# Kernel optimization log

Hardware: AMD Instinct MI355X
Metric: run time of the kernel (lower is better)

## Reference

```python
import jax, jax.numpy as jnp
import numpy as np

B, S, E, H = 4, 2048, 768, 12
D = E // H  # 64


def setup_inputs() -> dict:
    key = jax.random.key(0)
    ks = jax.random.split(key, 9)
    scale = 0.02
    return {
        "hidden_states": jax.random.normal(ks[0], (B, S, E), dtype=jnp.float32),
        "attention_mask": jax.random.normal(ks[1], (B, 1, 1, S), dtype=jnp.float32),
        "domain_attn_mask": jax.random.normal(ks[2], (B, 1, S, S), dtype=jnp.float32),
        "Wq": jax.random.normal(ks[3], (E, E), dtype=jnp.float32) * scale,
        "bq": jax.random.normal(ks[4], (E,), dtype=jnp.float32) * scale,
        "Wk": jax.random.normal(ks[5], (E, E), dtype=jnp.float32) * scale,
        "bk": jax.random.normal(ks[6], (E,), dtype=jnp.float32) * scale,
        "Wv": jax.random.normal(ks[7], (E, E), dtype=jnp.float32) * scale,
        "bv": jax.random.normal(ks[8], (E,), dtype=jnp.float32) * scale,
    }


def _split_heads(x):
    # [B,S,E] -> [B,H,S,D]
    b, s, _ = x.shape
    return x.reshape(b, s, H, D).transpose(0, 2, 1, 3)


def reference(hidden_states, attention_mask, domain_attn_mask, Wq, bq, Wk, bk, Wv, bv):
    # nn.Linear applies x @ W.T + b
    q = _split_heads(hidden_states @ Wq.T + bq)  # [B,H,S,D]
    k = _split_heads(hidden_states @ Wk.T + bk)
    v = _split_heads(hidden_states @ Wv.T + bv)

    inv_sqrt_d = 1.0 / (D ** 0.5)
    scores = jnp.einsum('bhqd,bhkd->bhqk', q, k) * inv_sqrt_d  # [B,H,S,S]
    scores = scores + attention_mask + domain_attn_mask  # two additive masks
    probs = jax.nn.softmax(scores, axis=-1)  # dropout prob = 0.0 (eval)
    ctx = jnp.einsum('bhqk,bhkd->bhqd', probs, v)  # [B,H,S,D]
    ctx = ctx.transpose(0, 2, 1, 3).reshape(hidden_states.shape[0], hidden_states.shape[1], E)
    return ctx
```

## Files before the change

### kernel.cpp

```cpp
#include <hip/hip_runtime.h>


typedef __bf16 bf16x8 __attribute__((ext_vector_type(8)));
typedef float f32x4 __attribute__((ext_vector_type(4)));
typedef unsigned short u16x8 __attribute__((ext_vector_type(8)));

#define MFMA16(a, b, c) __builtin_amdgcn_mfma_f32_16x16x32_bf16((a), (b), (c), 0, 0, 0)

__device__ __forceinline__ unsigned short f32_to_bf16(float f) {
    unsigned int u = __builtin_bit_cast(unsigned int, f);
    u += 0x7FFFu + ((u >> 16) & 1u);
    return (unsigned short)(u >> 16);
}

__device__ __forceinline__ void gload_lds16(const void* g, void* l) {
    __builtin_amdgcn_global_load_lds(
        (const __attribute__((address_space(1))) void*)g,
        (__attribute__((address_space(3))) void*)l, 16, 0, 0);
}

__global__ __launch_bounds__(256) void cvt_f32_bf16(const float* __restrict__ src,
                                                    unsigned short* __restrict__ dst, int n4) {
    int i = blockIdx.x * 256 + threadIdx.x;
    if (i < n4) {
        const float4 v = reinterpret_cast<const float4*>(src)[i];
        ushort4 o;
        o.x = f32_to_bf16(v.x);
        o.y = f32_to_bf16(v.y);
        o.z = f32_to_bf16(v.z);
        o.w = f32_to_bf16(v.w);
        reinterpret_cast<ushort4*>(dst)[i] = o;
    }
}

__global__ __launch_bounds__(256) void cvt_weights(const float* __restrict__ Wq,
                                                   const float* __restrict__ Wk,
                                                   const float* __restrict__ Wv,
                                                   unsigned short* __restrict__ Wb) {
    int i = blockIdx.x * 256 + threadIdx.x;
    const float* src;
    int local = i;
    if (i < 147456) {
        src = Wq;
    } else if (i < 294912) {
        src = Wk; local = i - 147456;
    } else {
        src = Wv; local = i - 294912;
    }
    const float4 v = reinterpret_cast<const float4*>(src)[local];
    ushort4 o;
    o.x = f32_to_bf16(v.x);
    o.y = f32_to_bf16(v.y);
    o.z = f32_to_bf16(v.z);
    o.w = f32_to_bf16(v.w);
    reinterpret_cast<ushort4*>(Wb)[i] = o;
}

__global__ __launch_bounds__(256) void qkv_gemm(const unsigned short* __restrict__ Xb,
                                                const unsigned short* __restrict__ Wb,
                                                const float* __restrict__ bq,
                                                const float* __restrict__ bk,
                                                const float* __restrict__ bv,
                                                unsigned short* __restrict__ Qb,
                                                unsigned short* __restrict__ Kb,
                                                unsigned short* __restrict__ Vb) {
    const int K = 768;
    __shared__ __align__(16) unsigned short Abuf[128 * 32];
    __shared__ __align__(16) unsigned short Bbuf[128 * 32];

    const int lane = threadIdx.x & 63;
    const int w    = threadIdx.x >> 6;
    const int col  = lane & 15;
    const int g    = lane >> 4;
    const int m0 = blockIdx.y * 128;
    const int n0 = blockIdx.x * 128;
    const int wm = w >> 1, wn = w & 1;

    const int srow = w * 16 + (lane >> 2);
    const int scol = (lane & 3) * 8;
    const unsigned short* gA0 = Xb + (size_t)(m0 + srow) * K + scol;
    const unsigned short* gA1 = gA0 + (size_t)64 * K;
    const unsigned short* gB0 = Wb + (size_t)(n0 + srow) * K + scol;
    const unsigned short* gB1 = gB0 + (size_t)64 * K;
    char* lA0 = (char*)Abuf + w * 1024;
    char* lA1 = (char*)Abuf + 4096 + w * 1024;
    char* lB0 = (char*)Bbuf + w * 1024;
    char* lB1 = (char*)Bbuf + 4096 + w * 1024;

    f32x4 acc[4][4] = {};
    for (int k0 = 0; k0 < K; k0 += 32) {
        __syncthreads();
        gload_lds16(gA0 + k0, lA0);
        gload_lds16(gA1 + k0, lA1);
        gload_lds16(gB0 + k0, lB0);
        gload_lds16(gB1 + k0, lB1);
        __syncthreads();
        bf16x8 a[4], bfr[4];
#pragma unroll
        for (int t = 0; t < 4; ++t) {
            a[t]   = *reinterpret_cast<const bf16x8*>(Abuf + (wm * 64 + t * 16 + col) * 32 + 8 * g);
            bfr[t] = *reinterpret_cast<const bf16x8*>(Bbuf + (wn * 64 + t * 16 + col) * 32 + 8 * g);
        }
#pragma unroll
        for (int mi = 0; mi < 4; ++mi)
#pragma unroll
            for (int ni = 0; ni < 4; ++ni)
                acc[mi][ni] = MFMA16(a[mi], bfr[ni], acc[mi][ni]);
    }

    const int which = n0 / 768;
    const float* bias = (which == 0) ? bq : (which == 1) ? bk : bv;
    const float scale = (which == 0) ? 0.125f : 1.0f;
    unsigned short* dst = (which == 0) ? Qb : (which == 1) ? Kb : Vb;

#pragma unroll
    for (int ni = 0; ni < 4; ++ni) {
        const int n = n0 + wn * 64 + ni * 16 + col;
        const int e = n - which * 768;
        const int h = e >> 6;
        const int d = e & 63;
        const float bb = bias[e];
#pragma unroll
        for (int mi = 0; mi < 4; ++mi)
#pragma unroll
            for (int i = 0; i < 4; ++i) {
                const int m   = m0 + wm * 64 + mi * 16 + 4 * g + i;
                const int bh  = (m >> 11) * 12 + h;
                const int srw = m & 2047;
                const float v = (acc[mi][ni][i] + bb) * scale;
                dst[((size_t)bh * 2048 + srw) * 64 + d] = f32_to_bf16(v);
            }
    }
}

__global__ __launch_bounds__(256) void transpose_v(const unsigned short* __restrict__ Vb,
                                                   unsigned short* __restrict__ Vt) {
    __shared__ unsigned short T[64][72];
    const int bh = blockIdx.y;
    const int s0 = blockIdx.x * 64;
    const int t  = threadIdx.x;
    const int r  = t >> 2;
    const int c0 = (t & 3) * 16;

    const unsigned short* src = Vb + ((size_t)bh * 2048 + s0 + r) * 64 + c0;
    u16x8 a = *reinterpret_cast<const u16x8*>(src);
    u16x8 b = *reinterpret_cast<const u16x8*>(src + 8);
#pragma unroll
    for (int j = 0; j < 8; ++j) {
        T[c0 + j][r]     = a[j];
        T[c0 + 8 + j][r] = b[j];
    }
    __syncthreads();
    unsigned short* dstp = Vt + ((size_t)bh * 64 + r) * 2048 + s0 + c0;
    *reinterpret_cast<u16x8*>(dstp)     = *reinterpret_cast<const u16x8*>(&T[r][c0]);
    *reinterpret_cast<u16x8*>(dstp + 8) = *reinterpret_cast<const u16x8*>(&T[r][c0 + 8]);
}

__global__ __launch_bounds__(256, 3) void attn_kernel(const unsigned short* __restrict__ Qb,
                                                      const unsigned short* __restrict__ Kb,
                                                      const unsigned short* __restrict__ Vt,
                                                      const float* __restrict__ amask,
                                                      const float* __restrict__ dmask,
                                                      float* __restrict__ out) {
    const int S = 2048, H = 12;
    const int lane = threadIdx.x & 63;
    const int w    = threadIdx.x >> 6;
    const int col  = lane & 15;
    const int g    = lane >> 4;

    const int phys    = blockIdx.x;
    const int logical = (phys & 7) * 96 + (phys >> 3);
    const int bh = logical >> 4;
    const int qt = logical & 15;
    const int b  = bh / H;
    const int h  = bh % H;
    const int q0 = qt * 128 + w * 32;

    __shared__ __align__(16) unsigned short Kl[2][4096];
    __shared__ __align__(16) unsigned short Vl[2][4096];
    __shared__ __align__(16) unsigned short Pl[4][32][72];

    bf16x8 qf[2][2];
#pragma unroll
    for (int qg = 0; qg < 2; ++qg)
#pragma unroll
        for (int kst = 0; kst < 2; ++kst)
            qf[qg][kst] = *reinterpret_cast<const bf16x8*>(
                Qb + ((size_t)bh * S + q0 + qg * 16 + col) * 64 + kst * 32 + 8 * g);

    f32x4 octx[2][4] = {};
    float m_run[2] = {-1e30f, -1e30f}, l_run[2] = {0.0f, 0.0f};

    const float* dmr0 = dmask + (size_t)b * S * S + (size_t)(q0 + col) * S;
    const float* dmr1 = dmr0 + (size_t)16 * S;
    const float* amr  = amask + (size_t)b * S;

#define STAGE(buf, KV)                                                              \
    {                                                                               \
        _Pragma("unroll")                                                           \
        for (int c = 0; c < 2; ++c) {                                               \
            const int base = w * 2048 + c * 1024;                      \
            const int o    = base + (lane << 4);                                    \
            const int row  = o >> 7;                                                \
            const int slot = (o >> 4) & 7;                                          \
            const int chunk = slot ^ (row & 7);                                     \
            gload_lds16((const char*)(Kb + ((size_t)bh * S + (KV) + row) * 64) + chunk * 16, \
                        (char*)&Kl[buf][0] + base);                                 \
            gload_lds16((const char*)(Vt + ((size_t)bh * 64 + row) * S + (KV)) + chunk * 16, \
                        (char*)&Vl[buf][0] + base);                                 \
        }                                                                           \
    }

    STAGE(0, 0)
    __syncthreads();

    int cur = 0;
    for (int t = 0; t < 32; ++t) {
        const int kv = t * 64;
        if (t + 1 < 32) STAGE(cur ^ 1, kv + 64)

        f32x4 dm[2][4], am4[4];
#pragma unroll
        for (int s = 0; s < 4; ++s) {
            dm[0][s] = *reinterpret_cast<const f32x4*>(dmr0 + kv + s * 16 + 4 * g);
            dm[1][s] = *reinterpret_cast<const f32x4*>(dmr1 + kv + s * 16 + 4 * g);
            am4[s]   = *reinterpret_cast<const f32x4*>(amr  + kv + s * 16 + 4 * g);
        }

        f32x4 sc[2][4] = {};
#pragma unroll
        for (int s = 0; s < 4; ++s) {
            const int row = s * 16 + col;
#pragma unroll
            for (int kst = 0; kst < 2; ++kst) {
                bf16x8 kf = *reinterpret_cast<const bf16x8*>(
                    (const char*)&Kl[cur][0] + row * 128 + (((g + 4 * kst) ^ (col & 7)) << 4));
                sc[0][s] = MFMA16(kf, qf[0][kst], sc[0][s]);
                sc[1][s] = MFMA16(kf, qf[1][kst], sc[1][s]);
            }
        }

#pragma unroll
        for (int qg = 0; qg < 2; ++qg) {
#pragma unroll
            for (int s = 0; s < 4; ++s) sc[qg][s] += dm[qg][s] + am4[s];
            float tm = sc[qg][0][0];
#pragma unroll
            for (int s = 0; s < 4; ++s)
#pragma unroll
                for (int i = 0; i < 4; ++i) tm = fmaxf(tm, sc[qg][s][i]);
            tm = fmaxf(tm, __shfl_xor(tm, 16));
            tm = fmaxf(tm, __shfl_xor(tm, 32));
            const bool grow = tm > m_run[qg];
            const float mn = fmaxf(m_run[qg], tm);
            float rs = 0.0f;
#pragma unroll
            for (int s = 0; s < 4; ++s)
#pragma unroll
                for (int i = 0; i < 4; ++i) {
                    const float p = __expf(sc[qg][s][i] - mn);
                    sc[qg][s][i] = p;
                    rs += p;
                }
            rs += __shfl_xor(rs, 16);
            rs += __shfl_xor(rs, 32);
            if (__any(grow)) {
                const float sf = __expf(m_run[qg] - mn);
                l_run[qg] = l_run[qg] * sf + rs;
                m_run[qg] = mn;
#pragma unroll
                for (int ds_ = 0; ds_ < 4; ++ds_) octx[qg][ds_] *= sf;
            } else {
                l_run[qg] += rs;
            }
#pragma unroll
            for (int s = 0; s < 4; ++s) {
                ushort4 u;
                u.x = f32_to_bf16(sc[qg][s][0]);
                u.y = f32_to_bf16(sc[qg][s][1]);
                u.z = f32_to_bf16(sc[qg][s][2]);
                u.w = f32_to_bf16(sc[qg][s][3]);
                *reinterpret_cast<ushort4*>(&Pl[w][qg * 16 + col][s * 16 + 4 * g]) = u;
            }
        }

        bf16x8 pb[2][2];
#pragma unroll
        for (int qg = 0; qg < 2; ++qg)
#pragma unroll
            for (int kst = 0; kst < 2; ++kst)
                pb[qg][kst] = *reinterpret_cast<const bf16x8*>(
                    &Pl[w][qg * 16 + col][kst * 32 + 8 * g]);
#pragma unroll
        for (int ds_ = 0; ds_ < 4; ++ds_) {
            const int row = ds_ * 16 + col;
#pragma unroll
            for (int kst = 0; kst < 2; ++kst) {
                bf16x8 vf = *reinterpret_cast<const bf16x8*>(
                    (const char*)&Vl[cur][0] + row * 128 + (((g + 4 * kst) ^ (col & 7)) << 4));
                octx[0][ds_] = MFMA16(vf, pb[0][kst], octx[0][ds_]);
                octx[1][ds_] = MFMA16(vf, pb[1][kst], octx[1][ds_]);
            }
        }

        __syncthreads();
        cur ^= 1;
    }

#pragma unroll
    for (int qg = 0; qg < 2; ++qg) {
        const float inv = 1.0f / l_run[qg];
        const size_t ob = ((size_t)b * S + q0 + qg * 16 + col) * 768 + h * 64;
#pragma unroll
        for (int ds_ = 0; ds_ < 4; ++ds_) {
            f32x4 o = octx[qg][ds_] * inv;
            *reinterpret_cast<f32x4*>(out + ob + ds_ * 16 + 4 * g) = o;
        }
    }
#undef STAGE
}

extern "C" void kernel_launch(void* const* d_in, const int* in_sizes, int n_in,
                              void* d_out, int out_size, void* d_ws, size_t ws_size,
                              hipStream_t stream) {
    const float* hidden = (const float*)d_in[0];
    const float* amask  = (const float*)d_in[1];
    const float* dmask  = (const float*)d_in[2];
    const float* Wq     = (const float*)d_in[3];
    const float* bq     = (const float*)d_in[4];
    const float* Wk     = (const float*)d_in[5];
    const float* bk     = (const float*)d_in[6];
    const float* Wv     = (const float*)d_in[7];
    const float* bv     = (const float*)d_in[8];
    float* out = (float*)d_out;

    unsigned short* Xb = (unsigned short*)d_ws;
    unsigned short* Wb = Xb + 6291456;
    unsigned short* Qb = Wb + 1769472;
    unsigned short* Kb = Qb + 6291456;
    unsigned short* Vb = Kb + 6291456;
    unsigned short* Vt = Xb;

    cvt_f32_bf16<<<6144, 256, 0, stream>>>(hidden, Xb, 1572864);
    cvt_weights<<<1728, 256, 0, stream>>>(Wq, Wk, Wv, Wb);
    qkv_gemm<<<dim3(18, 64), 256, 0, stream>>>(Xb, Wb, bq, bk, bv, Qb, Kb, Vb);
    transpose_v<<<dim3(32, 48), 256, 0, stream>>>(Vb, Vt);
    attn_kernel<<<768, 256, 0, stream>>>(Qb, Kb, Vt, amask, dmask, out);
}
```

Before: 318.1 us.

## Rework attention to 8 waves per block with exp2 softmax and deeper GEMM K tile

The attention kernel now runs 8 waves of 16 query rows each instead of 4 waves of 32, which lowers registers per wave and raises occupancy. Softmax uses a raw v_exp_f32 in base 2: log2(e) is folded into the Q scale and the mask add. MFMA sections are wrapped in s_setprio. The QKV GEMM moves to a 64-wide K tile with XOR-swizzled LDS to halve barriers and reduce bank conflicts. Each wave now reuses every loaded K/V fragment for half as many MFMAs, so LDS read traffic per MFMA rises.

Result: slower. 362.6 us (+14.0%).

```diff
diff --git a/kernel.cpp b/kernel.cpp
--- a/kernel.cpp
+++ b/kernel.cpp
@@ -2,10 +2,17 @@
 
 
 typedef __bf16 bf16x8 __attribute__((ext_vector_type(8)));
+typedef __bf16 bf16x4 __attribute__((ext_vector_type(4)));
 typedef float f32x4 __attribute__((ext_vector_type(4)));
 typedef unsigned short u16x8 __attribute__((ext_vector_type(8)));
 
 #define MFMA16(a, b, c) __builtin_amdgcn_mfma_f32_16x16x32_bf16((a), (b), (c), 0, 0, 0)
+
+__device__ __forceinline__ float exp2_fast(float x) {
+    float r;
+    asm("v_exp_f32 %0, %1" : "=v"(r) : "v"(x));
+    return r;
+}
 
 __device__ __forceinline__ unsigned short f32_to_bf16(float f) {
     unsigned int u = __builtin_bit_cast(unsigned int, f);
@@ -65,8 +72,8 @@
                                                 unsigned short* __restrict__ Kb,
                                                 unsigned short* __restrict__ Vb) {
     const int K = 768;
-    __shared__ __align__(16) unsigned short Abuf[128 * 32];
-    __shared__ __align__(16) unsigned short Bbuf[128 * 32];
+    __shared__ __align__(16) unsigned short Abuf[128 * 64];
+    __shared__ __align__(16) unsigned short Bbuf[128 * 64];
 
     const int lane = threadIdx.x & 63;
     const int w    = threadIdx.x >> 6;
@@ -76,41 +83,43 @@
     const int n0 = blockIdx.x * 128;
     const int wm = w >> 1, wn = w & 1;
 
-    const int srow = w * 16 + (lane >> 2);
-    const int scol = (lane & 3) * 8;
-    const unsigned short* gA0 = Xb + (size_t)(m0 + srow) * K + scol;
-    const unsigned short* gA1 = gA0 + (size_t)64 * K;
-    const unsigned short* gB0 = Wb + (size_t)(n0 + srow) * K + scol;
-    const unsigned short* gB1 = gB0 + (size_t)64 * K;
-    char* lA0 = (char*)Abuf + w * 1024;
-    char* lA1 = (char*)Abuf + 4096 + w * 1024;
-    char* lB0 = (char*)Bbuf + w * 1024;
-    char* lB1 = (char*)Bbuf + 4096 + w * 1024;
+    const int lrow   = lane >> 3;
+    const int lchunk = (lane & 7) ^ (lrow & 7);
+    const unsigned short* gA = Xb + (size_t)(m0 + w * 32 + lrow) * K + lchunk * 8;
+    const unsigned short* gB = Wb + (size_t)(n0 + w * 32 + lrow) * K + lchunk * 8;
 
     f32x4 acc[4][4] = {};
-    for (int k0 = 0; k0 < K; k0 += 32) {
+    for (int k0 = 0; k0 < K; k0 += 64) {
         __syncthreads();
-        gload_lds16(gA0 + k0, lA0);
-        gload_lds16(gA1 + k0, lA1);
-        gload_lds16(gB0 + k0, lB0);
-        gload_lds16(gB1 + k0, lB1);
+#pragma unroll
+        for (int c = 0; c < 4; ++c) {
+            gload_lds16(gA + (size_t)(c * 8) * K + k0, (char*)Abuf + w * 4096 + c * 1024);
+            gload_lds16(gB + (size_t)(c * 8) * K + k0, (char*)Bbuf + w * 4096 + c * 1024);
+        }
         __syncthreads();
-        bf16x8 a[4], bfr[4];
-#pragma unroll
-        for (int t = 0; t < 4; ++t) {
-            a[t]   = *reinterpret_cast<const bf16x8*>(Abuf + (wm * 64 + t * 16 + col) * 32 + 8 * g);
-            bfr[t] = *reinterpret_cast<const bf16x8*>(Bbuf + (wn * 64 + t * 16 + col) * 32 + 8 * g);
-        }
-#pragma unroll
-        for (int mi = 0; mi < 4; ++mi)
-#pragma unroll
-            for (int ni = 0; ni < 4; ++ni)
-                acc[mi][ni] = MFMA16(a[mi], bfr[ni], acc[mi][ni]);
+#pragma unroll
+        for (int kst = 0; kst < 2; ++kst) {
+            bf16x8 a[4], bfr[4];
+#pragma unroll
+            for (int t = 0; t < 4; ++t) {
+                const int ra = wm * 64 + t * 16 + col;
+                const int rb = wn * 64 + t * 16 + col;
+                a[t]   = *reinterpret_cast<const bf16x8*>(
+                    (const char*)Abuf + ra * 128 + (((g + 4 * kst) ^ (ra & 7)) << 4));
+                bfr[t] = *reinterpret_cast<const bf16x8*>(
+                    (const char*)Bbuf + rb * 128 + (((g + 4 * kst) ^ (rb & 7)) << 4));
+            }
+#pragma unroll
+            for (int mi = 0; mi < 4; ++mi)
+#pragma unroll
+                for (int ni = 0; ni < 4; ++ni)
+                    acc[mi][ni] = MFMA16(a[mi], bfr[ni], acc[mi][ni]);
+        }
     }
 
     const int which = n0 / 768;
     const float* bias = (which == 0) ? bq : (which == 1) ? bk : bv;
-    const float scale = (which == 0) ? 0.125f : 1.0f;
+    const float scale = (which == 0) ? 0.18033688011112042f : 1.0f;
     unsigned short* dst = (which == 0) ? Qb : (which == 1) ? Kb : Vb;
 
 #pragma unroll
@@ -156,13 +165,14 @@
     *reinterpret_cast<u16x8*>(dstp + 8) = *reinterpret_cast<const u16x8*>(&T[r][c0 + 8]);
 }
 
-__global__ __launch_bounds__(256, 3) void attn_kernel(const unsigned short* __restrict__ Qb,
+__global__ __launch_bounds__(512, 6) void attn_kernel(const unsigned short* __restrict__ Qb,
                                                       const unsigned short* __restrict__ Kb,
                                                       const unsigned short* __restrict__ Vt,
                                                       const float* __restrict__ amask,
                                                       const float* __restrict__ dmask,
                                                       float* __restrict__ out) {
     const int S = 2048, H = 12;
+    const float L2E = 1.4426950408889634f;
     const int lane = threadIdx.x & 63;
     const int w    = threadIdx.x >> 6;
     const int col  = lane & 15;
@@ -174,41 +184,36 @@
     const int qt = logical & 15;
     const int b  = bh / H;
     const int h  = bh % H;
-    const int q0 = qt * 128 + w * 32;
+    const int q0 = qt * 128 + w * 16;
+    const int q  = q0 + col;
 
     __shared__ __align__(16) unsigned short Kl[2][4096];
     __shared__ __align__(16) unsigned short Vl[2][4096];
-    __shared__ __align__(16) unsigned short Pl[4][32][72];
-
-    bf16x8 qf[2][2];
-#pragma unroll
-    for (int qg = 0; qg < 2; ++qg)
-#pragma unroll
-        for (int kst = 0; kst < 2; ++kst)
-            qf[qg][kst] = *reinterpret_cast<const bf16x8*>(
-                Qb + ((size_t)bh * S + q0 + qg * 16 + col) * 64 + kst * 32 + 8 * g);
-
-    f32x4 octx[2][4] = {};
-    float m_run[2] = {-1e30f, -1e30f}, l_run[2] = {0.0f, 0.0f};
-
-    const float* dmr0 = dmask + (size_t)b * S * S + (size_t)(q0 + col) * S;
-    const float* dmr1 = dmr0 + (size_t)16 * S;
-    const float* amr  = amask + (size_t)b * S;
-
+    __shared__ __align__(16) unsigned short Pl[8][16][72];
+
+    bf16x8 qf[2];
+#pragma unroll
+    for (int kst = 0; kst < 2; ++kst)
+        qf[kst] = *reinterpret_cast<const bf16x8*>(
+            Qb + ((size_t)bh * S + q) * 64 + kst * 32 + 8 * g);
+
+    f32x4 octx[4] = {};
+    float m_run = -1e30f, l_run = 0.0f;
+
+    const float* dmr = dmask + (size_t)b * S * S + (size_t)q * S;
+    const float* amr = amask + (size_t)b * S;
+
+    const int lrow   = lane >> 3;
+    const int lchunk = (lane & 7) ^ (lrow & 7);
 #define STAGE(buf, KV)                                                              \
     {                                                                               \
-        _Pragma("unroll")                                                           \
-        for (int c = 0; c < 2; ++c) {                                               \
-            const int base = w * 2048 + c * 1024;                      \
-            const int o    = base + (lane << 4);                                    \
-            const int row  = o >> 7;                                                \
-            const int slot = (o >> 4) & 7;                                          \
-            const int chunk = slot ^ (row & 7);                                     \
-            gload_lds16((const char*)(Kb + ((size_t)bh * S + (KV) + row) * 64) + chunk * 16, \
-                        (char*)&Kl[buf][0] + base);                                 \
-            gload_lds16((const char*)(Vt + ((size_t)bh * 64 + row) * S + (KV)) + chunk * 16, \
-                        (char*)&Vl[buf][0] + base);                                 \
-        }                                                                           \
+        const int base = w * 1024;                                                  \
+        gload_lds16((const char*)(Kb + ((size_t)bh * S + (KV) + w * 8 + lrow) * 64) \
+                        + lchunk * 16,                                              \
+                    (char*)&Kl[buf][0] + base);                                     \
+        gload_lds16((const char*)(Vt + ((size_t)bh * 64 + w * 8 + lrow) * S + (KV)) \
+                        + lchunk * 16,                                              \
+                    (char*)&Vl[buf][0] + base);                                     \
     }
 
     STAGE(0, 0)
@@ -219,15 +224,13 @@
         const int kv = t * 64;
         if (t + 1 < 32) STAGE(cur ^ 1, kv + 64)
 
-        f32x4 dm[2][4], am4[4];
-#pragma unroll
-        for (int s = 0; s < 4; ++s) {
-            dm[0][s] = *reinterpret_cast<const f32x4*>(dmr0 + kv + s * 16 + 4 * g);
-            dm[1][s] = *reinterpret_cast<const f32x4*>(dmr1 + kv + s * 16 + 4 * g);
-            am4[s]   = *reinterpret_cast<const f32x4*>(amr  + kv + s * 16 + 4 * g);
-        }
-
-        f32x4 sc[2][4] = {};
+        f32x4 dm[4];
+#pragma unroll
+        for (int s = 0; s < 4; ++s)
+            dm[s] = *reinterpret_cast<const f32x4*>(dmr + kv + s * 16 + 4 * g);
+
+        f32x4 sc[4] = {};
+        __builtin_amdgcn_s_setprio(1);
 #pragma unroll
         for (int s = 0; s < 4; ++s) {
             const int row = s * 16 + col;
@@ -235,62 +238,60 @@
             for (int kst = 0; kst < 2; ++kst) {
                 bf16x8 kf = *reinterpret_cast<const bf16x8*>(
                     (const char*)&Kl[cur][0] + row * 128 + (((g + 4 * kst) ^ (col & 7)) << 4));
-                sc[0][s] = MFMA16(kf, qf[0][kst], sc[0][s]);
-                sc[1][s] = MFMA16(kf, qf[1][kst], sc[1][s]);
-            }
-        }
-
-#pragma unroll
-        for (int qg = 0; qg < 2; ++qg) {
-#pragma unroll
-            for (int s = 0; s < 4; ++s) sc[qg][s] += dm[qg][s] + am4[s];
-            float tm = sc[qg][0][0];
-#pragma unroll
-            for (int s = 0; s < 4; ++s)
-#pragma unroll
-                for (int i = 0; i < 4; ++i) tm = fmaxf(tm, sc[qg][s][i]);
-            tm = fmaxf(tm, __shfl_xor(tm, 16));
-            tm = fmaxf(tm, __shfl_xor(tm, 32));
-            const bool grow = tm > m_run[qg];
-            const float mn = fmaxf(m_run[qg], tm);
-            float rs = 0.0f;
-#pragma unroll
-            for (int s = 0; s < 4; ++s)
-#pragma unroll
-                for (int i = 0; i < 4; ++i) {
-                    const float p = __expf(sc[qg][s][i] - mn);
-                    sc[qg][s][i] = p;
-                    rs += p;
-                }
-            rs += __shfl_xor(rs, 16);
-            rs += __shfl_xor(rs, 32);
-            if (__any(grow)) {
-                const float sf = __expf(m_run[qg] - mn);
-                l_run[qg] = l_run[qg] * sf + rs;
-                m_run[qg] = mn;
-#pragma unroll
-                for (int ds_ = 0; ds_ < 4; ++ds_) octx[qg][ds_] *= sf;
-            } else {
-                l_run[qg] += rs;
-            }
-#pragma unroll
-            for (int s = 0; s < 4; ++s) {
-                ushort4 u;
-                u.x = f32_to_bf16(sc[qg][s][0]);
-                u.y = f32_to_bf16(sc[qg][s][1]);
-                u.z = f32_to_bf16(sc[qg][s][2]);
-                u.w = f32_to_bf16(sc[qg][s][3]);
-                *reinterpret_cast<ushort4*>(&Pl[w][qg * 16 + col][s * 16 + 4 * g]) = u;
-            }
-        }
-
-        bf16x8 pb[2][2];
-#pragma unroll
-        for (int qg = 0; qg < 2; ++qg)
-#pragma unroll
-            for (int kst = 0; kst < 2; ++kst)
-                pb[qg][kst] = *reinterpret_cast<const bf16x8*>(
-                    &Pl[w][qg * 16 + col][kst * 32 + 8 * g]);
+                sc[s] = MFMA16(kf, qf[kst], sc[s]);
+            }
+        }
+        __builtin_amdgcn_s_setprio(0);
+
+#pragma unroll
+        for (int s = 0; s < 4; ++s) {
+            f32x4 a4 = *reinterpret_cast<const f32x4*>(amr + kv + s * 16 + 4 * g);
+            sc[s] += (dm[s] + a4) * L2E;
+        }
+        float tm = sc[0][0];
+#pragma unroll
+        for (int s = 0; s < 4; ++s)
+#pragma unroll
+            for (int i = 0; i < 4; ++i) tm = fmaxf(tm, sc[s][i]);
+        tm = fmaxf(tm, __shfl_xor(tm, 16));
+        tm = fmaxf(tm, __shfl_xor(tm, 32));
+        const bool grow = tm > m_run;
+        const float mn = fmaxf(m_run, tm);
+        float rs = 0.0f;
+#pragma unroll
+        for (int s = 0; s < 4; ++s)
+#pragma unroll
+            for (int i = 0; i < 4; ++i) {
+                const float p = exp2_fast(sc[s][i] - mn);
+                sc[s][i] = p;
+                rs += p;
+            }
+        rs += __shfl_xor(rs, 16);
+        rs += __shfl_xor(rs, 32);
+        if (__any(grow)) {
+            const float sf = exp2_fast(m_run - mn);
+            l_run = l_run * sf + rs;
+            m_run = mn;
+#pragma unroll
+            for (int ds_ = 0; ds_ < 4; ++ds_) octx[ds_] *= sf;
+        } else {
+            l_run += rs;
+        }
+#pragma unroll
+        for (int s = 0; s < 4; ++s) {
+            bf16x4 p;
+            p[0] = (__bf16)sc[s][0];
+            p[1] = (__bf16)sc[s][1];
+            p[2] = (__bf16)sc[s][2];
+            p[3] = (__bf16)sc[s][3];
+            *reinterpret_cast<bf16x4*>(&Pl[w][col][s * 16 + 4 * g]) = p;
+        }
+
+        bf16x8 pb[2];
+#pragma unroll
+        for (int kst = 0; kst < 2; ++kst)
+            pb[kst] = *reinterpret_cast<const bf16x8*>(&Pl[w][col][kst * 32 + 8 * g]);
+        __builtin_amdgcn_s_setprio(1);
 #pragma unroll
         for (int ds_ = 0; ds_ < 4; ++ds_) {
             const int row = ds_ * 16 + col;
@@ -298,24 +299,21 @@
             for (int kst = 0; kst < 2; ++kst) {
                 bf16x8 vf = *reinterpret_cast<const bf16x8*>(
                     (const char*)&Vl[cur][0] + row * 128 + (((g + 4 * kst) ^ (col & 7)) << 4));
-                octx[0][ds_] = MFMA16(vf, pb[0][kst], octx[0][ds_]);
-                octx[1][ds_] = MFMA16(vf, pb[1][kst], octx[1][ds_]);
-            }
-        }
+                octx[ds_] = MFMA16(vf, pb[kst], octx[ds_]);
+            }
+        }
+        __builtin_amdgcn_s_setprio(0);
 
         __syncthreads();
         cur ^= 1;
     }
 
-#pragma unroll
-    for (int qg = 0; qg < 2; ++qg) {
-        const float inv = 1.0f / l_run[qg];
-        const size_t ob = ((size_t)b * S + q0 + qg * 16 + col) * 768 + h * 64;
-#pragma unroll
-        for (int ds_ = 0; ds_ < 4; ++ds_) {
-            f32x4 o = octx[qg][ds_] * inv;
-            *reinterpret_cast<f32x4*>(out + ob + ds_ * 16 + 4 * g) = o;
-        }
+    const float inv = 1.0f / l_run;
+    const size_t ob = ((size_t)b * S + q) * 768 + h * 64;
+#pragma unroll
+    for (int ds_ = 0; ds_ < 4; ++ds_) {
+        f32x4 o = octx[ds_] * inv;
+        *reinterpret_cast<f32x4*>(out + ob + ds_ * 16 + 4 * g) = o;
     }
 #undef STAGE
 }
@@ -345,5 +343,5 @@
     cvt_weights<<<1728, 256, 0, stream>>>(Wq, Wk, Wv, Wb);
     qkv_gemm<<<dim3(18, 64), 256, 0, stream>>>(Xb, Wb, bq, bk, bv, Qb, Kb, Vb);
     transpose_v<<<dim3(32, 48), 256, 0, stream>>>(Vb, Vt);
-    attn_kernel<<<768, 256, 0, stream>>>(Qb, Kb, Vt, amask, dmask, out);
-}
+    attn_kernel<<<768, 512, 0, stream>>>(Qb, Kb, Vt, amask, dmask, out);
+}
```
